# Kernel tuning notes

Hardware: AMD Instinct MI355X
Metric: run time of the kernel (lower is better)

Reference implementation:

```python
import jax, jax.numpy as jnp
import numpy as np

DIM = 128
N_NODES = 50000
N_EDGES = 625000


def setup_inputs() -> dict:
    key = jax.random.key(0)
    ks = jax.random.split(key, 6)
    X = jax.random.normal(ks[0], (N_NODES, DIM), dtype=jnp.float32)
    edge_index = jax.random.randint(ks[1], (2, N_EDGES), 0, N_NODES, dtype=jnp.int64)
    # Linear params, init like torch (uniform +/- 1/sqrt(dim))
    bound = 1.0 / np.sqrt(DIM)
    msg_w = jax.random.uniform(ks[2], (DIM, DIM), minval=-bound, maxval=bound, dtype=jnp.float32)
    msg_b = jax.random.uniform(ks[3], (DIM,), minval=-bound, maxval=bound, dtype=jnp.float32)
    lin_w = jax.random.uniform(ks[4], (DIM, DIM), minval=-bound, maxval=bound, dtype=jnp.float32)
    lin_b = jax.random.uniform(ks[5], (DIM,), minval=-bound, maxval=bound, dtype=jnp.float32)
    eps = jnp.asarray(0.0, dtype=jnp.float32)
    return {"X": X, "edge_index": edge_index, "eps": eps,
            "msg_w": msg_w, "msg_b": msg_b, "lin_w": lin_w, "lin_b": lin_b}


def reference(X, edge_index, eps, msg_w, msg_b, lin_w, lin_b):
    src, dst = edge_index[0], edge_index[1]
    # msg_lin(X) then gather at dst: (E, F)
    msg = (jnp.einsum('nf,gf->ng', X, msg_w) + msg_b)[dst]
    # scatter-add messages onto src nodes: (N, F)
    agg = jax.ops.segment_sum(msg, src, num_segments=X.shape[0])
    out = (1.0 + eps) * X + agg
    out = jnp.einsum('nf,gf->ng', out, lin_w) + lin_b
    return jax.nn.relu(out)
```

## Files before the change

kernel.cpp:

```cpp
#include <hip/hip_runtime.h>
#include <hip/hip_bf16.h>

#define NN 50000
#define NE 625000
#define DIM 128

#define NBKT 1563
#define NBKTP 1568
#define CAP 640
#define CHUNK 4096
#define NCHUNK ((NE + CHUNK - 1) / CHUNK)

#define XCAST_NB 6250
#define PREP_NB 65
#define SETUP_NB (NCHUNK + XCAST_NB + PREP_NB)

using fragAB = __attribute__((ext_vector_type(8))) short;
using fragC  = __attribute__((ext_vector_type(4))) float;

__device__ __forceinline__ unsigned short f2bf(float f) {
    unsigned int u = __float_as_uint(f);
    unsigned int r = u + 0x7FFFu + ((u >> 16) & 1u);
    return (unsigned short)(r >> 16);
}

__device__ __forceinline__ float bflo(unsigned v) { return __uint_as_float(v << 16); }
__device__ __forceinline__ float bfhi(unsigned v) { return __uint_as_float(v & 0xffff0000u); }

__global__ __launch_bounds__(256) void mega_setup(
    const float* __restrict__ X, const int* __restrict__ ei,
    const float* __restrict__ L, const float* __restrict__ W,
    const float* __restrict__ mb, const float* __restrict__ epsp,
    float* __restrict__ cb, unsigned short* __restrict__ Bh,
    unsigned short* __restrict__ Xbf,
    int* __restrict__ bucket_cursor, unsigned* __restrict__ staging) {
    __shared__ int cnt[NBKTP];
    __shared__ int base[NBKTP];
    __shared__ int gb[NBKTP];
    __shared__ int wsum[4];
    __shared__ unsigned staged[CHUNK];
    int blk = blockIdx.x;
    int t = threadIdx.x;

    if (blk >= NCHUNK) {
        int xb = blk - NCHUNK;
        if (xb < XCAST_NB) {
            int idx = (xb * 256 + t) * 4;
            float4 v = *(const float4*)(X + idx);
            uint2 p;
            p.x = (unsigned)f2bf(v.x) | ((unsigned)f2bf(v.y) << 16);
            p.y = (unsigned)f2bf(v.z) | ((unsigned)f2bf(v.w) << 16);
            *(uint2*)(Xbf + idx) = p;
        } else {
            int idx = (xb - XCAST_NB) * 256 + t;
            float scale = 1.0f + *epsp;
            if (idx < DIM * DIM) {
                int o = idx >> 7, g = idx & 127;
                float s = 0.f;
                for (int f = 0; f < DIM; f++) s += L[o * DIM + f] * W[f * DIM + g];
                Bh[o * 256 + 128 + g] = f2bf(s);
                Bh[o * 256 + g] = f2bf(L[o * DIM + g] * scale);
            } else if (idx < DIM * DIM + DIM) {
                int o = idx - DIM * DIM;
                float s = 0.f;
                for (int f = 0; f < DIM; f++) s += L[o * DIM + f] * mb[f];
                cb[o] = s;
            }
        }
        return;
    }

    int e0 = blk * CHUNK;
    int nthis = NE - e0; if (nthis > CHUNK) nthis = CHUNK;

    for (int i = t; i < NBKTP; i += 256) cnt[i] = 0;
    __syncthreads();

    unsigned pk[CHUNK / 256];
#pragma unroll
    for (int i = 0; i < CHUNK / 256; i++) {
        int e = e0 + i * 256 + t;
        if (e < NE) {
            int s = ei[e];
            int d = ei[NE + e];
            unsigned b = (unsigned)s >> 5;
            pk[i] = (b << 21) | ((unsigned)(s & 31) << 16) | (unsigned)d;
            atomicAdd(&cnt[b], 1);
        } else pk[i] = 0xFFFFFFFFu;
    }
    __syncthreads();

    int myb = t * 8;
    int s0 = 0;
    if (myb < NBKTP) {
#pragma unroll
        for (int i = 0; i < 8; i++) s0 += cnt[myb + i];
    }
    int lane = t & 63, w = t >> 6;
    int v = s0;
#pragma unroll
    for (int off = 1; off < 64; off <<= 1) {
        int u = __shfl_up(v, off);
        if (lane >= off) v += u;
    }
    if (lane == 63) wsum[w] = v;
    __syncthreads();
    int add = 0;
#pragma unroll
    for (int i = 0; i < 4; i++)
        if (i < w) add += wsum[i];
    int run = v + add - s0;
    if (myb < NBKTP) {
        for (int i = 0; i < 8; i++) {
            int b = myb + i;
            base[b] = run;
            int c = cnt[b];
            gb[b] = (b < NBKT && c > 0) ? atomicAdd(&bucket_cursor[b], c) : 0;
            run += c;
        }
    }
    __syncthreads();
    if (myb < NBKTP) {
        for (int i = 0; i < 8; i++) cnt[myb + i] = base[myb + i];
    }
    __syncthreads();

#pragma unroll
    for (int i = 0; i < CHUNK / 256; i++) {
        if (pk[i] != 0xFFFFFFFFu) {
            unsigned b = pk[i] >> 21;
            int pos = atomicAdd(&cnt[b], 1);
            staged[pos] = pk[i];
        }
    }
    __syncthreads();

    for (int idx = t; idx < nthis; idx += 256) {
        unsigned p = staged[idx];
        unsigned b = p >> 21;
        int pos = gb[b] + (idx - base[b]);
        if (pos >= 0 && pos < CAP) staging[(size_t)b * CAP + pos] = p;
    }
}

__global__ __launch_bounds__(256, 8) void gather_gemm(
    const int* __restrict__ bucket_cursor, const unsigned* __restrict__ staging,
    const unsigned short* __restrict__ Xbf, const unsigned short* __restrict__ Bh,
    const float* __restrict__ cb, const float* __restrict__ lin_b,
    float* __restrict__ out) {
    __shared__ unsigned sorted_[CAP];
    __shared__ int hcnt[32];
    __shared__ int hbase[32];
    __shared__ int cur[32];
    __shared__ unsigned short As[32 * 136];
    int t = threadIdx.x;
    int b = blockIdx.x;
    int cnt_b = bucket_cursor[b];
    if (cnt_b > CAP) cnt_b = CAP;

    unsigned r0 = 0xFFFFFFFFu, r1 = 0xFFFFFFFFu, r2 = 0xFFFFFFFFu;
    if (t < cnt_b) r0 = staging[(size_t)b * CAP + t];
    if (t + 256 < cnt_b) r1 = staging[(size_t)b * CAP + t + 256];
    if (t + 512 < cnt_b) r2 = staging[(size_t)b * CAP + t + 512];

    if (t < 32) hcnt[t] = 0;
    __syncthreads();
    if (r0 != 0xFFFFFFFFu) atomicAdd(&hcnt[(r0 >> 16) & 31], 1);
    if (r1 != 0xFFFFFFFFu) atomicAdd(&hcnt[(r1 >> 16) & 31], 1);
    if (r2 != 0xFFFFFFFFu) atomicAdd(&hcnt[(r2 >> 16) & 31], 1);
    __syncthreads();
    if (t < 32) {
        int c = hcnt[t];
        int v = c;
#pragma unroll
        for (int off = 1; off < 32; off <<= 1) {
            int u = __shfl_up(v, off);
            if (t >= off) v += u;
        }
        int ex = v - c;
        hbase[t] = ex;
        cur[t] = ex;
    }
    __syncthreads();
    if (r0 != 0xFFFFFFFFu) {
        int pos = atomicAdd(&cur[(r0 >> 16) & 31], 1);
        sorted_[pos] = r0;
    }
    if (r1 != 0xFFFFFFFFu) {
        int pos = atomicAdd(&cur[(r1 >> 16) & 31], 1);
        sorted_[pos] = r1;
    }
    if (r2 != 0xFFFFFFFFu) {
        int pos = atomicAdd(&cur[(r2 >> 16) & 31], 1);
        sorted_[pos] = r2;
    }
    __syncthreads();

    int wave = t >> 6, lane = t & 63;
    int q = lane >> 4, l16 = lane & 15;
    const uint4* __restrict__ X4 = (const uint4*)Xbf;
    for (int ni = 0; ni < 8; ni++) {
        int local = wave * 8 + ni;
        int node = b * 32 + local;
        if (node >= NN) continue;
        int start = hbase[local];
        int cnt = hcnt[local];
        float a0 = 0.f, a1 = 0.f, a2 = 0.f, a3 = 0.f;
        float a4 = 0.f, a5 = 0.f, a6 = 0.f, a7 = 0.f;
        for (int jx = q; jx < cnt; jx += 16) {
            int j1 = jx + 4, j2 = jx + 8, j3 = jx + 12;
            unsigned s0v = sorted_[start + jx];
            unsigned s1v = sorted_[start + (j1 < cnt ? j1 : 0)];
            unsigned s2v = sorted_[start + (j2 < cnt ? j2 : 0)];
            unsigned s3v = sorted_[start + (j3 < cnt ? j3 : 0)];
            int d0 = (int)(s0v & 0xFFFFu);
            int d1 = (j1 < cnt) ? (int)(s1v & 0xFFFFu) : NN;
            int d2 = (j2 < cnt) ? (int)(s2v & 0xFFFFu) : NN;
            int d3 = (j3 < cnt) ? (int)(s3v & 0xFFFFu) : NN;
            uint4 v0 = X4[(size_t)d0 * 16 + l16];
            uint4 v1 = X4[(size_t)d1 * 16 + l16];
            uint4 v2 = X4[(size_t)d2 * 16 + l16];
            uint4 v3 = X4[(size_t)d3 * 16 + l16];
            a0 += bflo(v0.x); a1 += bfhi(v0.x); a2 += bflo(v0.y); a3 += bfhi(v0.y);
            a4 += bflo(v0.z); a5 += bfhi(v0.z); a6 += bflo(v0.w); a7 += bfhi(v0.w);
            a0 += bflo(v1.x); a1 += bfhi(v1.x); a2 += bflo(v1.y); a3 += bfhi(v1.y);
            a4 += bflo(v1.z); a5 += bfhi(v1.z); a6 += bflo(v1.w); a7 += bfhi(v1.w);
            a0 += bflo(v2.x); a1 += bfhi(v2.x); a2 += bflo(v2.y); a3 += bfhi(v2.y);
            a4 += bflo(v2.z); a5 += bfhi(v2.z); a6 += bflo(v2.w); a7 += bfhi(v2.w);
            a0 += bflo(v3.x); a1 += bfhi(v3.x); a2 += bflo(v3.y); a3 += bfhi(v3.y);
            a4 += bflo(v3.z); a5 += bfhi(v3.z); a6 += bflo(v3.w); a7 += bfhi(v3.w);
        }
        a0 += __shfl_xor(a0, 16); a1 += __shfl_xor(a1, 16);
        a2 += __shfl_xor(a2, 16); a3 += __shfl_xor(a3, 16);
        a4 += __shfl_xor(a4, 16); a5 += __shfl_xor(a5, 16);
        a6 += __shfl_xor(a6, 16); a7 += __shfl_xor(a7, 16);
        a0 += __shfl_xor(a0, 32); a1 += __shfl_xor(a1, 32);
        a2 += __shfl_xor(a2, 32); a3 += __shfl_xor(a3, 32);
        a4 += __shfl_xor(a4, 32); a5 += __shfl_xor(a5, 32);
        a6 += __shfl_xor(a6, 32); a7 += __shfl_xor(a7, 32);
        if (q == 0) {
            uint4 p;
            p.x = (unsigned)f2bf(a0) | ((unsigned)f2bf(a1) << 16);
            p.y = (unsigned)f2bf(a2) | ((unsigned)f2bf(a3) << 16);
            p.z = (unsigned)f2bf(a4) | ((unsigned)f2bf(a5) << 16);
            p.w = (unsigned)f2bf(a6) | ((unsigned)f2bf(a7) << 16);
            *(uint4*)(As + local * 136 + l16 * 8) = p;
        }
    }
    __syncthreads();

    int m16 = lane & 15;
    int quad = lane >> 4;
    int waveM = (wave & 1) * 16;
    int waveN = (wave >> 1) * 64;

    fragC acc[4];
#pragma unroll
    for (int j = 0; j < 4; j++) acc[j] = (fragC){0.f, 0.f, 0.f, 0.f};

    int xr = b * 32 + waveM + m16;
    if (xr >= NN) xr = NN;
#pragma unroll
    for (int kc = 0; kc < 4; kc++) {
        fragAB a = *(const fragAB*)(Xbf + (size_t)xr * 128 + kc * 32 + quad * 8);
#pragma unroll
        for (int j = 0; j < 4; j++) {
            fragAB bf = *(const fragAB*)(Bh + (size_t)(waveN + j * 16 + m16) * 256 + kc * 32 + quad * 8);
            acc[j] = __builtin_amdgcn_mfma_f32_16x16x32_bf16(a, bf, acc[j], 0, 0, 0);
        }
    }
#pragma unroll
    for (int kc = 4; kc < 8; kc++) {
        fragAB a = *(const fragAB*)(As + (waveM + m16) * 136 + (kc - 4) * 32 + quad * 8);
#pragma unroll
        for (int j = 0; j < 4; j++) {
            fragAB bf = *(const fragAB*)(Bh + (size_t)(waveN + j * 16 + m16) * 256 + kc * 32 + quad * 8);
            acc[j] = __builtin_amdgcn_mfma_f32_16x16x32_bf16(a, bf, acc[j], 0, 0, 0);
        }
    }

#pragma unroll
    for (int j = 0; j < 4; j++) {
        int col = waveN + j * 16 + m16;
        float cbc = cb[col];
        float lbc = lin_b[col];
        int lr = waveM + quad * 4;
#pragma unroll
        for (int r = 0; r < 4; r++) {
            int row = lr + r;
            int node = b * 32 + row;
            if (node < NN) {
                float dg = (float)hcnt[row];
                float v = acc[j][r] + dg * cbc + lbc;
                out[(size_t)node * 128 + col] = fmaxf(v, 0.f);
            }
        }
    }
}

extern "C" void kernel_launch(void* const* d_in, const int* in_sizes, int n_in,
                              void* d_out, int out_size, void* d_ws, size_t ws_size,
                              hipStream_t stream) {
    const float* X = (const float*)d_in[0];
    const int* ei = (const int*)d_in[1];
    const float* epsp = (const float*)d_in[2];
    const float* msg_w = (const float*)d_in[3];
    const float* msg_b = (const float*)d_in[4];
    const float* lin_w = (const float*)d_in[5];
    const float* lin_b = (const float*)d_in[6];
    float* out = (float*)d_out;

    int* bucket_cursor = (int*)d_ws;
    unsigned* staging = (unsigned*)(bucket_cursor + NBKTP);
    float* cb = (float*)(staging + (size_t)NBKT * CAP);
    unsigned short* Bh = (unsigned short*)(cb + DIM);
    unsigned short* Xbf = Bh + 128 * 256;

    hipMemsetAsync(bucket_cursor, 0, NBKTP * sizeof(int), stream);
    hipMemsetAsync(Xbf + (size_t)NN * 128, 0, 128 * sizeof(unsigned short), stream);

    mega_setup<<<SETUP_NB, 256, 0, stream>>>(X, ei, lin_w, msg_w, msg_b, epsp, cb, Bh, Xbf,
                                             bucket_cursor, staging);
    gather_gemm<<<NBKT, 256, 0, stream>>>(bucket_cursor, staging, Xbf, Bh, cb, lin_b, out);
}
```

Baseline: 168.6 us.

## Stream per-wave edge range with prefetched gathers instead of per-node loops

The aggregation phase changes from looping over each of a wave's 8 nodes separately (16 lanes per row, 4 edges per lane group) to a single streaming pass over the wave's contiguous sorted edge range. Each lane now owns 2 features, and the loop gathers 8 rows per batch, double-buffered with a prefetch of the next 8. Node boundaries are detected on the fly, flushing the accumulator into shared memory, and the shared tile is zero-initialised up front so nodes with no edges stay correct. The edge-staging chunk size is also halved, producing more, smaller bucketing blocks. The streaming pass removes per-node loop overhead, idle lanes and cross-lane reductions, at the cost of narrower 4-byte loads per lane and a branchy flush.

```diff
diff --git a/kernel.cpp b/kernel.cpp
--- a/kernel.cpp
+++ b/kernel.cpp
@@ -8,7 +8,7 @@
 #define NBKT 1563
 #define NBKTP 1568
 #define CAP 640
-#define CHUNK 4096
+#define CHUNK 2048
 #define NCHUNK ((NE + CHUNK - 1) / CHUNK)
 
 #define XCAST_NB 6250
@@ -164,6 +164,7 @@
     if (t + 512 < cnt_b) r2 = staging[(size_t)b * CAP + t + 512];
 
     if (t < 32) hcnt[t] = 0;
+    for (int i = t; i < 32 * 136 / 8; i += 256) ((uint4*)As)[i] = (uint4){0, 0, 0, 0};
     __syncthreads();
     if (r0 != 0xFFFFFFFFu) atomicAdd(&hcnt[(r0 >> 16) & 31], 1);
     if (r1 != 0xFFFFFFFFu) atomicAdd(&hcnt[(r1 >> 16) & 31], 1);
@@ -197,54 +198,52 @@
     __syncthreads();
 
     int wave = t >> 6, lane = t & 63;
-    int q = lane >> 4, l16 = lane & 15;
-    const uint4* __restrict__ X4 = (const uint4*)Xbf;
-    for (int ni = 0; ni < 8; ni++) {
-        int local = wave * 8 + ni;
-        int node = b * 32 + local;
-        if (node >= NN) continue;
-        int start = hbase[local];
-        int cnt = hcnt[local];
-        float a0 = 0.f, a1 = 0.f, a2 = 0.f, a3 = 0.f;
-        float a4 = 0.f, a5 = 0.f, a6 = 0.f, a7 = 0.f;
-        for (int jx = q; jx < cnt; jx += 16) {
-            int j1 = jx + 4, j2 = jx + 8, j3 = jx + 12;
-            unsigned s0v = sorted_[start + jx];
-            unsigned s1v = sorted_[start + (j1 < cnt ? j1 : 0)];
-            unsigned s2v = sorted_[start + (j2 < cnt ? j2 : 0)];
-            unsigned s3v = sorted_[start + (j3 < cnt ? j3 : 0)];
-            int d0 = (int)(s0v & 0xFFFFu);
-            int d1 = (j1 < cnt) ? (int)(s1v & 0xFFFFu) : NN;
-            int d2 = (j2 < cnt) ? (int)(s2v & 0xFFFFu) : NN;
-            int d3 = (j3 < cnt) ? (int)(s3v & 0xFFFFu) : NN;
-            uint4 v0 = X4[(size_t)d0 * 16 + l16];
-            uint4 v1 = X4[(size_t)d1 * 16 + l16];
-            uint4 v2 = X4[(size_t)d2 * 16 + l16];
-            uint4 v3 = X4[(size_t)d3 * 16 + l16];
-            a0 += bflo(v0.x); a1 += bfhi(v0.x); a2 += bflo(v0.y); a3 += bfhi(v0.y);
-            a4 += bflo(v0.z); a5 += bfhi(v0.z); a6 += bflo(v0.w); a7 += bfhi(v0.w);
-            a0 += bflo(v1.x); a1 += bfhi(v1.x); a2 += bflo(v1.y); a3 += bfhi(v1.y);
-            a4 += bflo(v1.z); a5 += bfhi(v1.z); a6 += bflo(v1.w); a7 += bfhi(v1.w);
-            a0 += bflo(v2.x); a1 += bfhi(v2.x); a2 += bflo(v2.y); a3 += bfhi(v2.y);
-            a4 += bflo(v2.z); a5 += bfhi(v2.z); a6 += bflo(v2.w); a7 += bfhi(v2.w);
-            a0 += bflo(v3.x); a1 += bfhi(v3.x); a2 += bflo(v3.y); a3 += bfhi(v3.y);
-            a4 += bflo(v3.z); a5 += bfhi(v3.z); a6 += bflo(v3.w); a7 += bfhi(v3.w);
-        }
-        a0 += __shfl_xor(a0, 16); a1 += __shfl_xor(a1, 16);
-        a2 += __shfl_xor(a2, 16); a3 += __shfl_xor(a3, 16);
-        a4 += __shfl_xor(a4, 16); a5 += __shfl_xor(a5, 16);
-        a6 += __shfl_xor(a6, 16); a7 += __shfl_xor(a7, 16);
-        a0 += __shfl_xor(a0, 32); a1 += __shfl_xor(a1, 32);
-        a2 += __shfl_xor(a2, 32); a3 += __shfl_xor(a3, 32);
-        a4 += __shfl_xor(a4, 32); a5 += __shfl_xor(a5, 32);
-        a6 += __shfl_xor(a6, 32); a7 += __shfl_xor(a7, 32);
-        if (q == 0) {
-            uint4 p;
-            p.x = (unsigned)f2bf(a0) | ((unsigned)f2bf(a1) << 16);
-            p.y = (unsigned)f2bf(a2) | ((unsigned)f2bf(a3) << 16);
-            p.z = (unsigned)f2bf(a4) | ((unsigned)f2bf(a5) << 16);
-            p.w = (unsigned)f2bf(a6) | ((unsigned)f2bf(a7) << 16);
-            *(uint4*)(As + local * 136 + l16 * 8) = p;
+    {
+        int lo = hbase[wave * 8];
+        int hi = (wave < 3) ? hbase[wave * 8 + 8] : cnt_b;
+        if (lo < hi) {
+            unsigned fake = (sorted_[hi - 1] & 0x001F0000u) | (unsigned)NN;
+            int curlocal = (int)((sorted_[lo] >> 16) & 31);
+            float acc0 = 0.f, acc1 = 0.f;
+            unsigned rec[8], vv[8];
+#pragma unroll
+            for (int k = 0; k < 8; k++) {
+                int jj = lo + k;
+                rec[k] = (jj < hi) ? sorted_[jj] : fake;
+            }
+#pragma unroll
+            for (int k = 0; k < 8; k++)
+                vv[k] = *(const unsigned*)(Xbf + (size_t)(rec[k] & 0xFFFFu) * 128 + (lane << 1));
+            for (int jb = lo; jb < hi; jb += 8) {
+                unsigned rec2[8], vv2[8];
+                int nb = jb + 8;
+                if (nb < hi) {
+#pragma unroll
+                    for (int k = 0; k < 8; k++) {
+                        int jj = nb + k;
+                        rec2[k] = (jj < hi) ? sorted_[jj] : fake;
+                    }
+#pragma unroll
+                    for (int k = 0; k < 8; k++)
+                        vv2[k] = *(const unsigned*)(Xbf + (size_t)(rec2[k] & 0xFFFFu) * 128 + (lane << 1));
+                }
+#pragma unroll
+                for (int k = 0; k < 8; k++) {
+                    int l = (int)((rec[k] >> 16) & 31);
+                    if (l != curlocal) {
+                        unsigned p = (unsigned)f2bf(acc0) | ((unsigned)f2bf(acc1) << 16);
+                        *(unsigned*)(As + curlocal * 136 + (lane << 1)) = p;
+                        acc0 = 0.f; acc1 = 0.f;
+                        curlocal = l;
+                    }
+                    acc0 += bflo(vv[k]);
+                    acc1 += bfhi(vv[k]);
+                }
+#pragma unroll
+                for (int k = 0; k < 8; k++) { rec[k] = rec2[k]; vv[k] = vv2[k]; }
+            }
+            unsigned p = (unsigned)f2bf(acc0) | ((unsigned)f2bf(acc1) << 16);
+            *(unsigned*)(As + curlocal * 136 + (lane << 1)) = p;
         }
     }
     __syncthreads();
```

Measured after the change: 188.7 us. 11.9% more time.

## Replace block-local counting sort with direct global atomic binning

Applied to the files above, without the earlier changes.

Drops the per-chunk shared-memory histogram, scan and staged scatter in the setup kernel. Each edge now takes its slot in its bucket with one global atomicAdd and writes straight to staging. Bucket cursors are padded to a 16-int stride (64 bytes) to spread contention across cache lines. This removes the syncs and shared-memory work and lets many smaller blocks run, at the cost of about 625k contended global atomics and uncoalesced scattered writes.

```diff
diff --git a/kernel.cpp b/kernel.cpp
--- a/kernel.cpp
+++ b/kernel.cpp
@@ -8,12 +8,12 @@
 #define NBKT 1563
 #define NBKTP 1568
 #define CAP 640
-#define CHUNK 4096
-#define NCHUNK ((NE + CHUNK - 1) / CHUNK)
-
+#define CURSTRIDE 16
+
+#define BIN_NB 611
 #define XCAST_NB 6250
 #define PREP_NB 65
-#define SETUP_NB (NCHUNK + XCAST_NB + PREP_NB)
+#define SETUP_NB (BIN_NB + XCAST_NB + PREP_NB)
 
 using fragAB = __attribute__((ext_vector_type(8))) short;
 using fragC  = __attribute__((ext_vector_type(4))) float;
@@ -34,112 +34,49 @@
     float* __restrict__ cb, unsigned short* __restrict__ Bh,
     unsigned short* __restrict__ Xbf,
     int* __restrict__ bucket_cursor, unsigned* __restrict__ staging) {
-    __shared__ int cnt[NBKTP];
-    __shared__ int base[NBKTP];
-    __shared__ int gb[NBKTP];
-    __shared__ int wsum[4];
-    __shared__ unsigned staged[CHUNK];
     int blk = blockIdx.x;
     int t = threadIdx.x;
 
-    if (blk >= NCHUNK) {
-        int xb = blk - NCHUNK;
-        if (xb < XCAST_NB) {
-            int idx = (xb * 256 + t) * 4;
-            float4 v = *(const float4*)(X + idx);
-            uint2 p;
-            p.x = (unsigned)f2bf(v.x) | ((unsigned)f2bf(v.y) << 16);
-            p.y = (unsigned)f2bf(v.z) | ((unsigned)f2bf(v.w) << 16);
-            *(uint2*)(Xbf + idx) = p;
-        } else {
-            int idx = (xb - XCAST_NB) * 256 + t;
-            float scale = 1.0f + *epsp;
-            if (idx < DIM * DIM) {
-                int o = idx >> 7, g = idx & 127;
-                float s = 0.f;
-                for (int f = 0; f < DIM; f++) s += L[o * DIM + f] * W[f * DIM + g];
-                Bh[o * 256 + 128 + g] = f2bf(s);
-                Bh[o * 256 + g] = f2bf(L[o * DIM + g] * scale);
-            } else if (idx < DIM * DIM + DIM) {
-                int o = idx - DIM * DIM;
-                float s = 0.f;
-                for (int f = 0; f < DIM; f++) s += L[o * DIM + f] * mb[f];
-                cb[o] = s;
+    if (blk < BIN_NB) {
+        int e0 = blk * 1024;
+#pragma unroll
+        for (int i = 0; i < 4; i++) {
+            int e = e0 + i * 256 + t;
+            if (e < NE) {
+                int s = ei[e];
+                int d = ei[NE + e];
+                unsigned b = (unsigned)s >> 5;
+                unsigned rec = (b << 21) | ((unsigned)(s & 31) << 16) | (unsigned)d;
+                int pos = atomicAdd(&bucket_cursor[b * CURSTRIDE], 1);
+                if (pos < CAP) staging[(size_t)b * CAP + pos] = rec;
             }
         }
         return;
     }
 
-    int e0 = blk * CHUNK;
-    int nthis = NE - e0; if (nthis > CHUNK) nthis = CHUNK;
-
-    for (int i = t; i < NBKTP; i += 256) cnt[i] = 0;
-    __syncthreads();
-
-    unsigned pk[CHUNK / 256];
-#pragma unroll
-    for (int i = 0; i < CHUNK / 256; i++) {
-        int e = e0 + i * 256 + t;
-        if (e < NE) {
-            int s = ei[e];
-            int d = ei[NE + e];
-            unsigned b = (unsigned)s >> 5;
-            pk[i] = (b << 21) | ((unsigned)(s & 31) << 16) | (unsigned)d;
-            atomicAdd(&cnt[b], 1);
-        } else pk[i] = 0xFFFFFFFFu;
-    }
-    __syncthreads();
-
-    int myb = t * 8;
-    int s0 = 0;
-    if (myb < NBKTP) {
-#pragma unroll
-        for (int i = 0; i < 8; i++) s0 += cnt[myb + i];
-    }
-    int lane = t & 63, w = t >> 6;
-    int v = s0;
-#pragma unroll
-    for (int off = 1; off < 64; off <<= 1) {
-        int u = __shfl_up(v, off);
-        if (lane >= off) v += u;
-    }
-    if (lane == 63) wsum[w] = v;
-    __syncthreads();
-    int add = 0;
-#pragma unroll
-    for (int i = 0; i < 4; i++)
-        if (i < w) add += wsum[i];
-    int run = v + add - s0;
-    if (myb < NBKTP) {
-        for (int i = 0; i < 8; i++) {
-            int b = myb + i;
-            base[b] = run;
-            int c = cnt[b];
-            gb[b] = (b < NBKT && c > 0) ? atomicAdd(&bucket_cursor[b], c) : 0;
-            run += c;
-        }
-    }
-    __syncthreads();
-    if (myb < NBKTP) {
-        for (int i = 0; i < 8; i++) cnt[myb + i] = base[myb + i];
-    }
-    __syncthreads();
-
-#pragma unroll
-    for (int i = 0; i < CHUNK / 256; i++) {
-        if (pk[i] != 0xFFFFFFFFu) {
-            unsigned b = pk[i] >> 21;
-            int pos = atomicAdd(&cnt[b], 1);
-            staged[pos] = pk[i];
-        }
-    }
-    __syncthreads();
-
-    for (int idx = t; idx < nthis; idx += 256) {
-        unsigned p = staged[idx];
-        unsigned b = p >> 21;
-        int pos = gb[b] + (idx - base[b]);
-        if (pos >= 0 && pos < CAP) staging[(size_t)b * CAP + pos] = p;
+    int xb = blk - BIN_NB;
+    if (xb < XCAST_NB) {
+        int idx = (xb * 256 + t) * 4;
+        float4 v = *(const float4*)(X + idx);
+        uint2 p;
+        p.x = (unsigned)f2bf(v.x) | ((unsigned)f2bf(v.y) << 16);
+        p.y = (unsigned)f2bf(v.z) | ((unsigned)f2bf(v.w) << 16);
+        *(uint2*)(Xbf + idx) = p;
+    } else {
+        int idx = (xb - XCAST_NB) * 256 + t;
+        float scale = 1.0f + *epsp;
+        if (idx < DIM * DIM) {
+            int o = idx >> 7, g = idx & 127;
+            float s = 0.f;
+            for (int f = 0; f < DIM; f++) s += L[o * DIM + f] * W[f * DIM + g];
+            Bh[o * 256 + 128 + g] = f2bf(s);
+            Bh[o * 256 + g] = f2bf(L[o * DIM + g] * scale);
+        } else if (idx < DIM * DIM + DIM) {
+            int o = idx - DIM * DIM;
+            float s = 0.f;
+            for (int f = 0; f < DIM; f++) s += L[o * DIM + f] * mb[f];
+            cb[o] = s;
+        }
     }
 }
 
@@ -155,7 +92,7 @@
     __shared__ unsigned short As[32 * 136];
     int t = threadIdx.x;
     int b = blockIdx.x;
-    int cnt_b = bucket_cursor[b];
+    int cnt_b = bucket_cursor[b * CURSTRIDE];
     if (cnt_b > CAP) cnt_b = CAP;
 
     unsigned r0 = 0xFFFFFFFFu, r1 = 0xFFFFFFFFu, r2 = 0xFFFFFFFFu;
@@ -311,12 +248,12 @@
     float* out = (float*)d_out;
 
     int* bucket_cursor = (int*)d_ws;
-    unsigned* staging = (unsigned*)(bucket_cursor + NBKTP);
+    unsigned* staging = (unsigned*)(bucket_cursor + NBKTP * CURSTRIDE);
     float* cb = (float*)(staging + (size_t)NBKT * CAP);
     unsigned short* Bh = (unsigned short*)(cb + DIM);
     unsigned short* Xbf = Bh + 128 * 256;
 
-    hipMemsetAsync(bucket_cursor, 0, NBKTP * sizeof(int), stream);
+    hipMemsetAsync(bucket_cursor, 0, NBKTP * CURSTRIDE * sizeof(int), stream);
     hipMemsetAsync(Xbf + (size_t)NN * 128, 0, 128 * sizeof(unsigned short), stream);
 
     mega_setup<<<SETUP_NB, 256, 0, stream>>>(X, ei, lin_w, msg_w, msg_b, epsp, cb, Bh, Xbf,
```

Result: slower. 172.4 us (+2.2%).
